# Performance work log

Hardware: AMD Instinct MI355X
Metric: run time of the kernel (lower is better)

Reference implementation:

```python
import jax, jax.numpy as jnp
import numpy as np

GAMMA = 1.0
BIG = 1e8  # boundary sentinel, matches 100000000.0 in the original


def _softdtw_R(D, gamma=GAMMA):
    """Forward soft-DTW DP. D: [N, M] distance matrix -> R: [N, M].
    R[i,j] = D[i,j] + softmin_gamma(R[i-1,j-1], R[i-1,j], R[i,j-1])."""
    N, M = D.shape
    dt = D.dtype

    def row_step(prev_row, d_row):
        # prev_row: [M+1] = padded previous row R[i-1, 0..M] (index 0 = left boundary)
        diag = prev_row[:-1]  # R[i-1, j-1]
        up = prev_row[1:]     # R[i-1, j]

        def cell(r_left, xs):
            dg, u, d = xs
            z = jnp.stack([dg, u, r_left]) * (-1.0 / gamma)
            m = jnp.max(z)
            softmin = -gamma * (jnp.log(jnp.sum(jnp.exp(z - m))) + m)
            r = d + softmin
            return r, r

        _, row = jax.lax.scan(cell, jnp.asarray(BIG, dt), (diag, up, d_row))
        new_prev = jnp.concatenate([jnp.full((1,), BIG, dt), row])
        return new_prev, row

    # padded row 0: corner R[0,0]=0, top boundary = BIG
    init = jnp.concatenate([jnp.zeros((1,), dt), jnp.full((M,), BIG, dt)])
    _, R = jax.lax.scan(row_step, init, D)
    return R  # [N, M]


def reference(x):
    # x: [B, N, M, 1] batch of distance matrices
    D = jnp.squeeze(x, axis=-1)
    R = jax.vmap(_softdtw_R)(D)
    return R[..., None]  # [B, N, M, 1]


def setup_inputs() -> dict:
    key = jax.random.key(0)
    B, N, M = 32, 512, 512
    x = jax.random.uniform(key, (B, N, M, 1), dtype=jnp.float32)
    return {"x": x}
```

## Files before the change

### kernel.cpp

```cpp
#include <hip/hip_runtime.h>

#define N_DIM 512
#define M_DIM 512
#define NQUAD 128
#define TSTEPS 192
#define DEPTH 4
#define SLOT_BYTES 8192
#define RING_BYTES (DEPTH * SLOT_BYTES)
#define BSTRIDE (N_DIM * M_DIM)
#define GSTRIDE (NQUAD * 64)
#define ROW_BYTES 2048
#define ROW_MAX (511 * 2048)
#define LN2F 0.6931471805599453f

#define AS1 __attribute__((address_space(1)))
#define AS3 __attribute__((address_space(3)))

__global__ __launch_bounds__(256) void exp_pre(const float4* __restrict__ D4,
                                               float4* __restrict__ E4, int n4) {
    int i = blockIdx.x * blockDim.x + threadIdx.x;
    const int stride = gridDim.x * blockDim.x;
    for (; i < n4; i += stride) {
        const float4 v = D4[i];
        E4[i] = make_float4(__expf(-v.x), __expf(-v.y), __expf(-v.z), __expf(-v.w));
    }
}

__global__ __launch_bounds__(256) void log_post(float4* __restrict__ E4,
                                                const float* __restrict__ gm, int n4) {
    int i = blockIdx.x * blockDim.x + threadIdx.x;
    const int stride = gridDim.x * blockDim.x;
    for (; i < n4; i += stride) {
        const int b   = i >> 16;
        const int rem = i & 65535;
        const int row = rem >> 7;
        const int c4  = rem & 127;
        const float g = gm[(b << 13) + ((row >> 2) << 6) + (c4 >> 1)];
        const float4 v = E4[i];
        E4[i] = make_float4(g - __logf(v.x), g - __logf(v.y),
                            g - __logf(v.z), g - __logf(v.w));
    }
}

__device__ inline float shup1(float x) {
    int r = __builtin_amdgcn_update_dpp(0, __float_as_int(x), 0x138, 0xf, 0xf, true);
    return __int_as_float(r);
}
__device__ inline int shup1i(int x) {
    return __builtin_amdgcn_update_dpp(0, x, 0x138, 0xf, 0xf, true);
}
__device__ inline int fr_exp(float x) {
    int e; asm("v_frexp_exp_i32_f32 %0, %1" : "=v"(e) : "v"(x)); return e;
}
__device__ inline float ldx(float x, int k) {
    float r; asm("v_ldexp_f32 %0, %1, %2" : "=v"(r) : "v"(x), "v"(k)); return r;
}

template<bool PRE>
__global__ __launch_bounds__(64, 1) void softdtw_dp(const float* __restrict__ Dsrc,
                                                    float* __restrict__ Eout,
                                                    float* __restrict__ gmap) {
    const int b     = blockIdx.x;
    const int l     = threadIdx.x;
    const int laneB = l << 5;

    const float* __restrict__ Db = Dsrc + (size_t)b * BSTRIDE;
    float*       __restrict__ Rb = Eout + (size_t)b * BSTRIDE;
    float*       __restrict__ gm = gmap + (size_t)b * GSTRIDE;

    __shared__ char ring[RING_BYTES] __attribute__((aligned(16)));
    const unsigned ring_base = (unsigned)(size_t)(AS3 char*)ring;

    auto EV = [&](float v) -> float { return PRE ? v : __expf(-v); };

    float Ep[8];
    #pragma unroll
    for (int k = 0; k < 8; ++k) Ep[k] = 0.0f;
    float fQ = 0.0f;
    int   KG = 0;
    int   KE = 0;
    int   Kh = 0;
    float expA7 = 0.0f, expB7 = 0.0f, expC7 = 0.0f, expD7 = 0.0f;
    float E7hD = 0.0f;

    int raw[4];
    #pragma unroll
    for (int k = 0; k < 4; ++k) raw[k] = (16 + k) * ROW_BYTES - (l << 13);
    int soff = -(l << 13);

    float4 P[8], Nx[8];
    #pragma unroll
    for (int row = 0; row < 4; ++row) {
        const int r = min(max(-4 * l + row, 0), N_DIM - 1);
        P[2 * row]     = *(const float4*)(Db + (size_t)r * M_DIM + (l << 3));
        P[2 * row + 1] = *(const float4*)(Db + (size_t)r * M_DIM + (l << 3) + 4);
    }
    #pragma unroll
    for (int sig = 1; sig < DEPTH; ++sig) {
        const unsigned wo = (unsigned)sig * SLOT_BYTES;
        #pragma unroll
        for (int k = 0; k < 4; ++k) {
            const int cl = min(max((4 * (sig - l) + k) * ROW_BYTES, 0), ROW_MAX);
            const char* gp = (const char*)Db + cl + laneB;
            __builtin_amdgcn_global_load_lds((const AS1 void*)gp,
                                             (AS3 void*)(ring + wo + (2 * k) * 1024), 16, 0, 0);
            __builtin_amdgcn_global_load_lds((const AS1 void*)(gp + 16),
                                             (AS3 void*)(ring + wo + (2 * k + 1) * 1024), 16, 0, 0);
        }
    }
    asm volatile("s_waitcnt vmcnt(0)" ::: "memory");

    auto rowfma = [&](const float* endv, float eLeft, const float* Q, float* E) {
        float e = eLeft;
        #pragma unroll
        for (int c = 0; c < 8; ++c) {
            e = __builtin_fmaf(endv[c], e, endv[c] * Q[c]);
            E[c] = e;
        }
    };

    auto step = [&](int s, float4 (&cur)[8], float4 (&nxt)[8]) {
        {
            const unsigned wo = ((unsigned)(s + DEPTH) & (DEPTH - 1)) * SLOT_BYTES;
            #pragma unroll
            for (int k = 0; k < 4; ++k) {
                const int cl = min(max(raw[k], 0), ROW_MAX);
                const char* gp = (const char*)Db + cl + laneB;
                __builtin_amdgcn_global_load_lds((const AS1 void*)gp,
                                                 (AS3 void*)(ring + wo + (2 * k) * 1024), 16, 0, 0);
                __builtin_amdgcn_global_load_lds((const AS1 void*)(gp + 16),
                                                 (AS3 void*)(ring + wo + (2 * k + 1) * 1024), 16, 0, 0);
                raw[k] += 4 * ROW_BYTES;
            }
        }
        asm volatile("s_waitcnt vmcnt(51)" ::: "memory");

        const float E7sA = shup1(expA7);
        const float E7sB = shup1(expB7);
        const float E7sC = shup1(expC7);
        const float E7sD = shup1(expD7);
        const int   Ks   = shup1i(KE);

        const unsigned raddr = ring_base
                             + (unsigned)((s + 1) & (DEPTH - 1)) * SLOT_BYTES
                             + (unsigned)l * 16u;
        asm volatile("ds_read_b128 %0, %8 offset:0\n\t"
                     "ds_read_b128 %1, %8 offset:1024\n\t"
                     "ds_read_b128 %2, %8 offset:2048\n\t"
                     "ds_read_b128 %3, %8 offset:3072\n\t"
                     "ds_read_b128 %4, %8 offset:4096\n\t"
                     "ds_read_b128 %5, %8 offset:5120\n\t"
                     "ds_read_b128 %6, %8 offset:6144\n\t"
                     "ds_read_b128 %7, %8 offset:7168"
                     : "=&v"(nxt[0]), "=&v"(nxt[1]), "=&v"(nxt[2]), "=&v"(nxt[3]),
                       "=&v"(nxt[4]), "=&v"(nxt[5]), "=&v"(nxt[6]), "=&v"(nxt[7])
                     : "v"(raddr));

        const int t = s - l;
        if (t >= 0 && t < NQUAD) {
            const float endA[8] = {EV(cur[0].x), EV(cur[0].y), EV(cur[0].z), EV(cur[0].w),
                                   EV(cur[1].x), EV(cur[1].y), EV(cur[1].z), EV(cur[1].w)};
            const float endB[8] = {EV(cur[2].x), EV(cur[2].y), EV(cur[2].z), EV(cur[2].w),
                                   EV(cur[3].x), EV(cur[3].y), EV(cur[3].z), EV(cur[3].w)};
            const float endC[8] = {EV(cur[4].x), EV(cur[4].y), EV(cur[4].z), EV(cur[4].w),
                                   EV(cur[5].x), EV(cur[5].y), EV(cur[5].z), EV(cur[5].w)};
            const float endD[8] = {EV(cur[6].x), EV(cur[6].y), EV(cur[6].z), EV(cur[6].w),
                                   EV(cur[7].x), EV(cur[7].y), EV(cur[7].z), EV(cur[7].w)};

            const bool is0    = (t == 0);
            const bool origin = is0 && (l == 0);
            int K = is0 ? (Ks - fr_exp(E7sA)) : KG;
            K = origin ? 0 : K;
            const float fq = is0 ? 0.0f : fQ;
            const int dKs = K - Ks;
            const int dKh = K - Kh;

            const float eLA = ldx(E7sA, dKs);
            const float eLB = ldx(E7sB, dKs);
            const float eLC = ldx(E7sC, dKs);
            const float eLD = ldx(E7sD, dKs);
            float eDA0 = ldx(E7hD, dKh);
            eDA0 = is0 ? 0.0f : eDA0;
            eDA0 = origin ? 1.0f : eDA0;

            float QA[8];
            QA[0] = eDA0 + fq * Ep[0];
            #pragma unroll
            for (int c = 1; c < 8; ++c) QA[c] = fq * (Ep[c - 1] + Ep[c]);
            float EA[8];
            rowfma(endA, eLA, QA, EA);

            float QB[8];
            QB[0] = eLA + EA[0];
            #pragma unroll
            for (int c = 1; c < 8; ++c) QB[c] = EA[c - 1] + EA[c];
            float EB[8];
            rowfma(endB, eLB, QB, EB);

            float QC[8];
            QC[0] = eLB + EB[0];
            #pragma unroll
            for (int c = 1; c < 8; ++c) QC[c] = EB[c - 1] + EB[c];
            float EC[8];
            rowfma(endC, eLC, QC, EC);

            float QD[8];
            QD[0] = eLC + EC[0];
            #pragma unroll
            for (int c = 1; c < 8; ++c) QD[c] = EC[c - 1] + EC[c];
            float ED[8];
            rowfma(endD, eLD, QD, ED);

            char* sb  = (char*)Rb + soff + laneB;
            char* sb2 = sb + 4096;
            *(float4*)(sb)         = make_float4(EA[0], EA[1], EA[2], EA[3]);
            *(float4*)(sb + 16)    = make_float4(EA[4], EA[5], EA[6], EA[7]);
            *(float4*)(sb + 2048)  = make_float4(EB[0], EB[1], EB[2], EB[3]);
            *(float4*)(sb + 2064)  = make_float4(EB[4], EB[5], EB[6], EB[7]);
            *(float4*)(sb2)        = make_float4(EC[0], EC[1], EC[2], EC[3]);
            *(float4*)(sb2 + 16)   = make_float4(EC[4], EC[5], EC[6], EC[7]);
            *(float4*)(sb2 + 2048) = make_float4(ED[0], ED[1], ED[2], ED[3]);
            *(float4*)(sb2 + 2064) = make_float4(ED[4], ED[5], ED[6], ED[7]);
            gm[(t << 6) + l] = (float)K * LN2F;

            const int ed = fr_exp(ED[0]);
            KG = K - ed;
            fQ = ldx(1.0f, -ed);
            KE = K;
            #pragma unroll
            for (int c = 0; c < 8; ++c) Ep[c] = ED[c];
            expA7 = EA[7]; expB7 = EB[7]; expC7 = EC[7]; expD7 = ED[7];
        }

        E7hD = E7sD;
        Kh   = Ks;
        soff += 4 * ROW_BYTES;

        asm volatile("s_waitcnt lgkmcnt(0)" ::: "memory");
        __builtin_amdgcn_sched_barrier(0);
    };

    for (int s = 0; s < TSTEPS; s += 2) {
        step(s,     P,  Nx);
        step(s + 1, Nx, P);
    }
}

extern "C" void kernel_launch(void* const* d_in, const int* in_sizes, int n_in,
                              void* d_out, int out_size, void* d_ws, size_t ws_size,
                              hipStream_t stream) {
    const float* x = (const float*)d_in[0];
    float* out     = (float*)d_out;
    const int B    = in_sizes[0] / BSTRIDE;
    const int n4   = (B * BSTRIDE) / 4;
    const size_t DEXP_BYTES = (size_t)B * BSTRIDE * sizeof(float);
    const size_t GMAP_BYTES = (size_t)B * GSTRIDE * sizeof(float);

    if (ws_size >= DEXP_BYTES + GMAP_BYTES) {
        float* dexp = (float*)d_ws;
        float* gm   = (float*)((char*)d_ws + DEXP_BYTES);
        exp_pre<<<dim3(2048), dim3(256), 0, stream>>>((const float4*)x, (float4*)dexp, n4);
        softdtw_dp<true><<<dim3(B), dim3(64), 0, stream>>>(dexp, out, gm);
        log_post<<<dim3(2048), dim3(256), 0, stream>>>((float4*)out, gm, n4);
    } else {
        float* gm = (float*)d_ws;
        softdtw_dp<false><<<dim3(B), dim3(64), 0, stream>>>(x, out, gm);
        log_post<<<dim3(2048), dim3(256), 0, stream>>>((float4*)out, gm, n4);
    }
}
```

Measured before the change: 135.5 us.

## Pre-skew input into anti-diagonal slot layout so DP loads and stores are contiguous

The pre-pass now applies exp and also rearranges D into one 8 KB slot per wavefront step, ordered by anti-diagonal. The DP kernel then streams each slot with contiguous global_load_lds and writes results to a matching skewed buffer. A new post-pass un-skews those results while applying the log and scale. This removes the strided, clamped per-lane row gathers and scattered stores from the latency-bound serial DP, at the cost of extra gather/scatter work in the parallel pre and post kernels and more workspace.

```diff
diff --git a/kernel.cpp b/kernel.cpp
--- a/kernel.cpp
+++ b/kernel.cpp
@@ -7,8 +7,11 @@
 #define DEPTH 4
 #define SLOT_BYTES 8192
 #define RING_BYTES (DEPTH * SLOT_BYTES)
+#define SIGMA_MAX (TSTEPS + DEPTH)
 #define BSTRIDE (N_DIM * M_DIM)
 #define GSTRIDE (NQUAD * 64)
+#define DSKEW_B ((size_t)SIGMA_MAX * SLOT_BYTES)
+#define ESKEW_B ((size_t)TSTEPS * SLOT_BYTES)
 #define ROW_BYTES 2048
 #define ROW_MAX (511 * 2048)
 #define LN2F 0.6931471805599453f
@@ -16,18 +19,40 @@
 #define AS1 __attribute__((address_space(1)))
 #define AS3 __attribute__((address_space(3)))
 
-__global__ __launch_bounds__(256) void exp_pre(const float4* __restrict__ D4,
-                                               float4* __restrict__ E4, int n4) {
-    int i = blockIdx.x * blockDim.x + threadIdx.x;
-    const int stride = gridDim.x * blockDim.x;
-    for (; i < n4; i += stride) {
-        const float4 v = D4[i];
-        E4[i] = make_float4(__expf(-v.x), __expf(-v.y), __expf(-v.z), __expf(-v.w));
-    }
-}
-
-__global__ __launch_bounds__(256) void log_post(float4* __restrict__ E4,
-                                                const float* __restrict__ gm, int n4) {
+__global__ __launch_bounds__(256) void skew_pre(const float* __restrict__ D,
+                                                char* __restrict__ Dsk) {
+    const int b  = blockIdx.y;
+    const int l  = threadIdx.x & 63;
+    const int cg = (blockIdx.x << 2) + (threadIdx.x >> 6);
+    const int sigma = cg >> 3;
+    const int chunk = cg & 7;
+    const int k = chunk >> 1, h = chunk & 1;
+    const int row = min(max(4 * (sigma - l) + k, 0), N_DIM - 1);
+    const float4 v = *(const float4*)(D + (size_t)b * BSTRIDE + (row << 9) + (l << 3) + (h << 2));
+    *(float4*)(Dsk + (size_t)b * DSKEW_B + (size_t)sigma * SLOT_BYTES + chunk * 1024 + (l << 4)) =
+        make_float4(__expf(-v.x), __expf(-v.y), __expf(-v.z), __expf(-v.w));
+}
+
+__global__ __launch_bounds__(256) void unskew_post(const char* __restrict__ Esk,
+                                                   const float* __restrict__ gm,
+                                                   float* __restrict__ R) {
+    const int b   = blockIdx.y;
+    const int idx = (blockIdx.x << 8) + threadIdx.x;
+    const int i   = idx >> 7;
+    const int j4  = idx & 127;
+    const int l = j4 >> 1, h = j4 & 1;
+    const int t = i >> 2,  k = i & 3;
+    const int sigma = t + l;
+    const int chunk = (k << 1) + h;
+    const float4 v = *(const float4*)(Esk + (size_t)b * ESKEW_B + (size_t)sigma * SLOT_BYTES
+                                      + chunk * 1024 + (l << 4));
+    const float g = gm[b * GSTRIDE + (t << 6) + l];
+    *(float4*)(R + (size_t)b * BSTRIDE + (i << 9) + (j4 << 2)) =
+        make_float4(g - __logf(v.x), g - __logf(v.y), g - __logf(v.z), g - __logf(v.w));
+}
+
+__global__ __launch_bounds__(256) void log_post_plain(float4* __restrict__ E4,
+                                                      const float* __restrict__ gm, int n4) {
     int i = blockIdx.x * blockDim.x + threadIdx.x;
     const int stride = gridDim.x * blockDim.x;
     for (; i < n4; i += stride) {
@@ -56,33 +81,197 @@
     float r; asm("v_ldexp_f32 %0, %1, %2" : "=v"(r) : "v"(x), "v"(k)); return r;
 }
 
-template<bool PRE>
-__global__ __launch_bounds__(64, 1) void softdtw_dp(const float* __restrict__ Dsrc,
-                                                    float* __restrict__ Eout,
-                                                    float* __restrict__ gmap) {
+__global__ __launch_bounds__(64, 1) void softdtw_dp_skew(const char* __restrict__ Dsk,
+                                                         char* __restrict__ Esk,
+                                                         float* __restrict__ gmap) {
+    const int b = blockIdx.x;
+    const int l = threadIdx.x;
+    const int laneB16 = l << 4;
+
+    const char* __restrict__ DskB = Dsk + (size_t)b * DSKEW_B;
+    char*       __restrict__ EskB = Esk + (size_t)b * ESKEW_B;
+    float*      __restrict__ gm   = gmap + (size_t)b * GSTRIDE;
+
+    __shared__ char ring[RING_BYTES] __attribute__((aligned(16)));
+    const unsigned ring_base = (unsigned)(size_t)(AS3 char*)ring;
+
+    float Ep[8];
+    #pragma unroll
+    for (int k = 0; k < 8; ++k) Ep[k] = 0.0f;
+    float fQ = 0.0f;
+    int   KG = 0, KE = 0, Kh = 0;
+    float expA7 = 0.0f, expB7 = 0.0f, expC7 = 0.0f, expD7 = 0.0f;
+    float E7hD = 0.0f;
+
+    int dsk_off = DEPTH * SLOT_BYTES;
+    int es_off  = 0;
+
+    float4 P[8], Nx[8];
+    #pragma unroll
+    for (int ch = 0; ch < 8; ++ch)
+        P[ch] = *(const float4*)(DskB + ch * 1024 + laneB16);
+    #pragma unroll
+    for (int sig = 1; sig < DEPTH; ++sig) {
+        const char* gp = DskB + sig * SLOT_BYTES + laneB16;
+        #pragma unroll
+        for (int ch = 0; ch < 8; ++ch)
+            __builtin_amdgcn_global_load_lds((const AS1 void*)(gp + ch * 1024),
+                                             (AS3 void*)(ring + sig * SLOT_BYTES + ch * 1024),
+                                             16, 0, 0);
+    }
+    asm volatile("s_waitcnt vmcnt(0)" ::: "memory");
+
+    auto rowfma = [&](const float* endv, float eLeft, const float* Q, float* E) {
+        float e = eLeft;
+        #pragma unroll
+        for (int c = 0; c < 8; ++c) {
+            e = __builtin_fmaf(endv[c], e, endv[c] * Q[c]);
+            E[c] = e;
+        }
+    };
+
+    auto step = [&](int s, float4 (&cur)[8], float4 (&nxt)[8]) {
+        {
+            const unsigned wo = ((unsigned)s & (DEPTH - 1)) * SLOT_BYTES;
+            const char* gp = DskB + dsk_off + laneB16;
+            #pragma unroll
+            for (int ch = 0; ch < 8; ++ch)
+                __builtin_amdgcn_global_load_lds((const AS1 void*)(gp + ch * 1024),
+                                                 (AS3 void*)(ring + wo + ch * 1024), 16, 0, 0);
+            dsk_off += SLOT_BYTES;
+        }
+        asm volatile("s_waitcnt vmcnt(51)" ::: "memory");
+
+        const float E7sA = shup1(expA7);
+        const float E7sB = shup1(expB7);
+        const float E7sC = shup1(expC7);
+        const float E7sD = shup1(expD7);
+        const int   Ks   = shup1i(KE);
+
+        const unsigned raddr = ring_base
+                             + (unsigned)((s + 1) & (DEPTH - 1)) * SLOT_BYTES
+                             + (unsigned)laneB16;
+        asm volatile("ds_read_b128 %0, %8 offset:0\n\t"
+                     "ds_read_b128 %1, %8 offset:1024\n\t"
+                     "ds_read_b128 %2, %8 offset:2048\n\t"
+                     "ds_read_b128 %3, %8 offset:3072\n\t"
+                     "ds_read_b128 %4, %8 offset:4096\n\t"
+                     "ds_read_b128 %5, %8 offset:5120\n\t"
+                     "ds_read_b128 %6, %8 offset:6144\n\t"
+                     "ds_read_b128 %7, %8 offset:7168"
+                     : "=&v"(nxt[0]), "=&v"(nxt[1]), "=&v"(nxt[2]), "=&v"(nxt[3]),
+                       "=&v"(nxt[4]), "=&v"(nxt[5]), "=&v"(nxt[6]), "=&v"(nxt[7])
+                     : "v"(raddr));
+
+        const int t = s - l;
+        if (t >= 0 && t < NQUAD) {
+            const float endA[8] = {cur[0].x, cur[0].y, cur[0].z, cur[0].w,
+                                   cur[1].x, cur[1].y, cur[1].z, cur[1].w};
+            const float endB[8] = {cur[2].x, cur[2].y, cur[2].z, cur[2].w,
+                                   cur[3].x, cur[3].y, cur[3].z, cur[3].w};
+            const float endC[8] = {cur[4].x, cur[4].y, cur[4].z, cur[4].w,
+                                   cur[5].x, cur[5].y, cur[5].z, cur[5].w};
+            const float endD[8] = {cur[6].x, cur[6].y, cur[6].z, cur[6].w,
+                                   cur[7].x, cur[7].y, cur[7].z, cur[7].w};
+
+            const bool is0    = (t == 0);
+            const bool origin = is0 && (l == 0);
+            int K = is0 ? (Ks - fr_exp(E7sA)) : KG;
+            K = origin ? 0 : K;
+            const float fq = is0 ? 0.0f : fQ;
+            const int dKs = K - Ks;
+            const int dKh = K - Kh;
+
+            const float eLA = ldx(E7sA, dKs);
+            const float eLB = ldx(E7sB, dKs);
+            const float eLC = ldx(E7sC, dKs);
+            const float eLD = ldx(E7sD, dKs);
+            float eDA0 = ldx(E7hD, dKh);
+            eDA0 = is0 ? 0.0f : eDA0;
+            eDA0 = origin ? 1.0f : eDA0;
+
+            float QA[8];
+            QA[0] = eDA0 + fq * Ep[0];
+            #pragma unroll
+            for (int c = 1; c < 8; ++c) QA[c] = fq * (Ep[c - 1] + Ep[c]);
+            float EA[8];
+            rowfma(endA, eLA, QA, EA);
+
+            float QB[8];
+            QB[0] = eLA + EA[0];
+            #pragma unroll
+            for (int c = 1; c < 8; ++c) QB[c] = EA[c - 1] + EA[c];
+            float EB[8];
+            rowfma(endB, eLB, QB, EB);
+
+            float QC[8];
+            QC[0] = eLB + EB[0];
+            #pragma unroll
+            for (int c = 1; c < 8; ++c) QC[c] = EB[c - 1] + EB[c];
+            float EC[8];
+            rowfma(endC, eLC, QC, EC);
+
+            float QD[8];
+            QD[0] = eLC + EC[0];
+            #pragma unroll
+            for (int c = 1; c < 8; ++c) QD[c] = EC[c - 1] + EC[c];
+            float ED[8];
+            rowfma(endD, eLD, QD, ED);
+
+            char* sb  = EskB + es_off + laneB16;
+            char* sb2 = sb + 4096;
+            *(float4*)(sb)         = make_float4(EA[0], EA[1], EA[2], EA[3]);
+            *(float4*)(sb + 1024)  = make_float4(EA[4], EA[5], EA[6], EA[7]);
+            *(float4*)(sb + 2048)  = make_float4(EB[0], EB[1], EB[2], EB[3]);
+            *(float4*)(sb + 3072)  = make_float4(EB[4], EB[5], EB[6], EB[7]);
+            *(float4*)(sb2)        = make_float4(EC[0], EC[1], EC[2], EC[3]);
+            *(float4*)(sb2 + 1024) = make_float4(EC[4], EC[5], EC[6], EC[7]);
+            *(float4*)(sb2 + 2048) = make_float4(ED[0], ED[1], ED[2], ED[3]);
+            *(float4*)(sb2 + 3072) = make_float4(ED[4], ED[5], ED[6], ED[7]);
+            gm[(t << 6) + l] = (float)K * LN2F;
+
+            const int ed = fr_exp(ED[0]);
+            KG = K - ed;
+            fQ = ldx(1.0f, -ed);
+            KE = K;
+            #pragma unroll
+            for (int c = 0; c < 8; ++c) Ep[c] = ED[c];
+            expA7 = EA[7]; expB7 = EB[7]; expC7 = EC[7]; expD7 = ED[7];
+        }
+
+        E7hD = E7sD;
+        Kh   = Ks;
+        es_off += SLOT_BYTES;
+
+        asm volatile("s_waitcnt lgkmcnt(0)" ::: "memory");
+        __builtin_amdgcn_sched_barrier(0);
+    };
+
+    for (int s = 0; s < TSTEPS; s += 2) {
+        step(s,     P,  Nx);
+        step(s + 1, Nx, P);
+    }
+}
+
+__global__ __launch_bounds__(64, 1) void softdtw_dp_direct(const float* __restrict__ Dsrc,
+                                                           float* __restrict__ Eout,
+                                                           float* __restrict__ gmap) {
     const int b     = blockIdx.x;
     const int l     = threadIdx.x;
     const int laneB = l << 5;
-
     const float* __restrict__ Db = Dsrc + (size_t)b * BSTRIDE;
     float*       __restrict__ Rb = Eout + (size_t)b * BSTRIDE;
     float*       __restrict__ gm = gmap + (size_t)b * GSTRIDE;
-
     __shared__ char ring[RING_BYTES] __attribute__((aligned(16)));
     const unsigned ring_base = (unsigned)(size_t)(AS3 char*)ring;
 
-    auto EV = [&](float v) -> float { return PRE ? v : __expf(-v); };
-
     float Ep[8];
     #pragma unroll
     for (int k = 0; k < 8; ++k) Ep[k] = 0.0f;
     float fQ = 0.0f;
-    int   KG = 0;
-    int   KE = 0;
-    int   Kh = 0;
+    int KG = 0, KE = 0, Kh = 0;
     float expA7 = 0.0f, expB7 = 0.0f, expC7 = 0.0f, expD7 = 0.0f;
     float E7hD = 0.0f;
-
     int raw[4];
     #pragma unroll
     for (int k = 0; k < 4; ++k) raw[k] = (16 + k) * ROW_BYTES - (l << 13);
@@ -134,13 +323,11 @@
             }
         }
         asm volatile("s_waitcnt vmcnt(51)" ::: "memory");
-
         const float E7sA = shup1(expA7);
         const float E7sB = shup1(expB7);
         const float E7sC = shup1(expC7);
         const float E7sD = shup1(expD7);
         const int   Ks   = shup1i(KE);
-
         const unsigned raddr = ring_base
                              + (unsigned)((s + 1) & (DEPTH - 1)) * SLOT_BYTES
                              + (unsigned)l * 16u;
@@ -155,18 +342,16 @@
                      : "=&v"(nxt[0]), "=&v"(nxt[1]), "=&v"(nxt[2]), "=&v"(nxt[3]),
                        "=&v"(nxt[4]), "=&v"(nxt[5]), "=&v"(nxt[6]), "=&v"(nxt[7])
                      : "v"(raddr));
-
         const int t = s - l;
         if (t >= 0 && t < NQUAD) {
-            const float endA[8] = {EV(cur[0].x), EV(cur[0].y), EV(cur[0].z), EV(cur[0].w),
-                                   EV(cur[1].x), EV(cur[1].y), EV(cur[1].z), EV(cur[1].w)};
-            const float endB[8] = {EV(cur[2].x), EV(cur[2].y), EV(cur[2].z), EV(cur[2].w),
-                                   EV(cur[3].x), EV(cur[3].y), EV(cur[3].z), EV(cur[3].w)};
-            const float endC[8] = {EV(cur[4].x), EV(cur[4].y), EV(cur[4].z), EV(cur[4].w),
-                                   EV(cur[5].x), EV(cur[5].y), EV(cur[5].z), EV(cur[5].w)};
-            const float endD[8] = {EV(cur[6].x), EV(cur[6].y), EV(cur[6].z), EV(cur[6].w),
-                                   EV(cur[7].x), EV(cur[7].y), EV(cur[7].z), EV(cur[7].w)};
-
+            const float endA[8] = {__expf(-cur[0].x), __expf(-cur[0].y), __expf(-cur[0].z), __expf(-cur[0].w),
+                                   __expf(-cur[1].x), __expf(-cur[1].y), __expf(-cur[1].z), __expf(-cur[1].w)};
+            const float endB[8] = {__expf(-cur[2].x), __expf(-cur[2].y), __expf(-cur[2].z), __expf(-cur[2].w),
+                                   __expf(-cur[3].x), __expf(-cur[3].y), __expf(-cur[3].z), __expf(-cur[3].w)};
+            const float endC[8] = {__expf(-cur[4].x), __expf(-cur[4].y), __expf(-cur[4].z), __expf(-cur[4].w),
+                                   __expf(-cur[5].x), __expf(-cur[5].y), __expf(-cur[5].z), __expf(-cur[5].w)};
+            const float endD[8] = {__expf(-cur[6].x), __expf(-cur[6].y), __expf(-cur[6].z), __expf(-cur[6].w),
+                                   __expf(-cur[7].x), __expf(-cur[7].y), __expf(-cur[7].z), __expf(-cur[7].w)};
             const bool is0    = (t == 0);
             const bool origin = is0 && (l == 0);
             int K = is0 ? (Ks - fr_exp(E7sA)) : KG;
@@ -174,7 +359,6 @@
             const float fq = is0 ? 0.0f : fQ;
             const int dKs = K - Ks;
             const int dKh = K - Kh;
-
             const float eLA = ldx(E7sA, dKs);
             const float eLB = ldx(E7sB, dKs);
             const float eLC = ldx(E7sC, dKs);
@@ -182,35 +366,26 @@
             float eDA0 = ldx(E7hD, dKh);
             eDA0 = is0 ? 0.0f : eDA0;
             eDA0 = origin ? 1.0f : eDA0;
-
             float QA[8];
             QA[0] = eDA0 + fq * Ep[0];
             #pragma unroll
             for (int c = 1; c < 8; ++c) QA[c] = fq * (Ep[c - 1] + Ep[c]);
-            float EA[8];
-            rowfma(endA, eLA, QA, EA);
-
+            float EA[8]; rowfma(endA, eLA, QA, EA);
             float QB[8];
             QB[0] = eLA + EA[0];
             #pragma unroll
             for (int c = 1; c < 8; ++c) QB[c] = EA[c - 1] + EA[c];
-            float EB[8];
-            rowfma(endB, eLB, QB, EB);
-
+            float EB[8]; rowfma(endB, eLB, QB, EB);
             float QC[8];
             QC[0] = eLB + EB[0];
             #pragma unroll
             for (int c = 1; c < 8; ++c) QC[c] = EB[c - 1] + EB[c];
-            float EC[8];
-            rowfma(endC, eLC, QC, EC);
-
+            float EC[8]; rowfma(endC, eLC, QC, EC);
             float QD[8];
             QD[0] = eLC + EC[0];
             #pragma unroll
             for (int c = 1; c < 8; ++c) QD[c] = EC[c - 1] + EC[c];
-            float ED[8];
-            rowfma(endD, eLD, QD, ED);
-
+            float ED[8]; rowfma(endD, eLD, QD, ED);
             char* sb  = (char*)Rb + soff + laneB;
             char* sb2 = sb + 4096;
             *(float4*)(sb)         = make_float4(EA[0], EA[1], EA[2], EA[3]);
@@ -222,7 +397,6 @@
             *(float4*)(sb2 + 2048) = make_float4(ED[0], ED[1], ED[2], ED[3]);
             *(float4*)(sb2 + 2064) = make_float4(ED[4], ED[5], ED[6], ED[7]);
             gm[(t << 6) + l] = (float)K * LN2F;
-
             const int ed = fr_exp(ED[0]);
             KG = K - ed;
             fQ = ldx(1.0f, -ed);
@@ -231,11 +405,9 @@
             for (int c = 0; c < 8; ++c) Ep[c] = ED[c];
             expA7 = EA[7]; expB7 = EB[7]; expC7 = EC[7]; expD7 = ED[7];
         }
-
         E7hD = E7sD;
         Kh   = Ks;
         soff += 4 * ROW_BYTES;
-
         asm volatile("s_waitcnt lgkmcnt(0)" ::: "memory");
         __builtin_amdgcn_sched_barrier(0);
     };
@@ -252,19 +424,20 @@
     const float* x = (const float*)d_in[0];
     float* out     = (float*)d_out;
     const int B    = in_sizes[0] / BSTRIDE;
-    const int n4   = (B * BSTRIDE) / 4;
-    const size_t DEXP_BYTES = (size_t)B * BSTRIDE * sizeof(float);
     const size_t GMAP_BYTES = (size_t)B * GSTRIDE * sizeof(float);
-
-    if (ws_size >= DEXP_BYTES + GMAP_BYTES) {
-        float* dexp = (float*)d_ws;
-        float* gm   = (float*)((char*)d_ws + DEXP_BYTES);
-        exp_pre<<<dim3(2048), dim3(256), 0, stream>>>((const float4*)x, (float4*)dexp, n4);
-        softdtw_dp<true><<<dim3(B), dim3(64), 0, stream>>>(dexp, out, gm);
-        log_post<<<dim3(2048), dim3(256), 0, stream>>>((float4*)out, gm, n4);
+    const size_t need_skew  = (size_t)B * (DSKEW_B + ESKEW_B) + GMAP_BYTES;
+
+    if (ws_size >= need_skew) {
+        char*  dsk = (char*)d_ws;
+        char*  esk = dsk + (size_t)B * DSKEW_B;
+        float* gm  = (float*)(esk + (size_t)B * ESKEW_B);
+        skew_pre<<<dim3(392, B), dim3(256), 0, stream>>>(x, dsk);
+        softdtw_dp_skew<<<dim3(B), dim3(64), 0, stream>>>(dsk, esk, gm);
+        unskew_post<<<dim3(256, B), dim3(256), 0, stream>>>(esk, gm, out);
     } else {
         float* gm = (float*)d_ws;
-        softdtw_dp<false><<<dim3(B), dim3(64), 0, stream>>>(x, out, gm);
-        log_post<<<dim3(2048), dim3(256), 0, stream>>>((float4*)out, gm, n4);
-    }
-}
+        const int n4 = (B * BSTRIDE) / 4;
+        softdtw_dp_direct<<<dim3(B), dim3(64), 0, stream>>>(x, out, gm);
+        log_post_plain<<<dim3(2048), dim3(256), 0, stream>>>((float4*)out, gm, n4);
+    }
+}
```

Measured after the change: 143.8 us. +6.2%, slower.
